# Optimization experiments

Hardware: AMD Instinct MI355X
Metric: run time of the kernel (lower is better)

The kernel has to match this reference:

```python
import jax, jax.numpy as jnp
import numpy as np

TAU = 0.3  # default tau in selectCom_adap
K = 1      # hard-coded K in selectCom_adap

B, C, N, M = 8, 64, 2048, 2048


def setup_inputs() -> dict:
    key = jax.random.key(0)
    k1, k2, k3, k4 = jax.random.split(key, 4)
    return {
        "src_emb": jax.random.normal(k1, (B, C, N), dtype=jnp.float32),
        "tgt_emb": jax.random.normal(k2, (B, C, M), dtype=jnp.float32),
        "src": jax.random.normal(k3, (B, 3, N), dtype=jnp.float32),
        "tgt": jax.random.normal(k4, (B, 3, M), dtype=jnp.float32),
    }


def reference(src_emb, tgt_emb, src, tgt):
    # EPCOR eval path: selectCom_adap + get_sparse_w
    dtype = src_emb.dtype
    Np = src_emb.shape[2]
    Mp = tgt_emb.shape[2]
    tgt_K = int(Mp * TAU)
    src_K = int(Np * TAU)

    inner = jnp.einsum('bcn,bcm->bnm', src_emb, tgt_emb)
    xx = jnp.sum(src_emb * src_emb, axis=1)[:, :, None]   # [B,N,1]
    yy = jnp.sum(tgt_emb * tgt_emb, axis=1)[:, None, :]   # [B,1,M]
    pd = 2.0 * inner - xx - yy                             # [B,N,M]

    # column softmax and tgt outlier mask (smallest tgt_K column mass)
    scoresSoftCol = jax.nn.softmax(pd, axis=2)
    scoresColSum = jnp.sum(scoresSoftCol, axis=1)          # [B,M]
    col_thresh = -jax.lax.top_k(-scoresColSum, tgt_K)[0][:, -1]  # tgt_K-th smallest, [B]
    mask_tgt = (scoresColSum < col_thresh[:, None])[:, None, :]  # [B,1,M]

    # row softmax and src outlier mask (smallest src_K row mass)
    scoresSoftRow = jax.nn.softmax(pd, axis=1)
    scoresRowSum = jnp.sum(scoresSoftRow, axis=2)          # [B,N]
    row_thresh = -jax.lax.top_k(-scoresRowSum, src_K)[0][:, -1]  # [B]
    mask_src = (scoresRowSum < row_thresh[:, None])[:, :, None]  # [B,N,1]

    mask = jnp.logical_or(mask_src, mask_tgt)              # [B,N,M]

    # torch precedence: mask = (mask + scoresSoftCol) < topk  (bool promoted to float)
    topk = jax.lax.top_k(scoresSoftCol, K)[0][..., -1:]    # K-th largest per row, [B,N,1]
    mask = (mask.astype(dtype) + scoresSoftCol) < topk     # [B,N,M]

    w_sparse = jnp.where(mask, jnp.zeros((), dtype), scoresSoftCol)
    colsum = jnp.sum(w_sparse, axis=-1, keepdims=True)
    colsum = jnp.where(colsum < 1e-5, jnp.asarray(1e-5, dtype), colsum)
    src_tgt_weight = w_sparse / colsum                     # row-renormalized sparse weights

    val_sum = jnp.sum(src_tgt_weight, axis=-1, keepdims=True)  # [B,N,1]
    val_sum_inlier = jnp.where(mask_src, jnp.zeros((), dtype), val_sum)[..., 0]  # [B,N]
    src_weight = val_sum_inlier / jnp.sum(val_sum_inlier, axis=-1, keepdims=True)

    # src_corr = tgt @ src_tgt_weight^T : [B,3,M] x [B,N,M] -> [B,3,N]
    src_corr = jnp.einsum('bdm,bnm->bdn', tgt, src_tgt_weight)
    return src_corr, src_weight, mask_src, mask_tgt
```

## Files before the change

### kernel.cpp

```cpp
#include <hip/hip_runtime.h>

#define BB 8
#define CC 64
#define NN 2048
#define MM 2048
#define KSEL 613
#define MT 32
#define MT2 16
#define NT2 16
#define NCH 16

#define OUT_W  (BB * 3 * NN)
#define OUT_MS (OUT_W + BB * NN)
#define OUT_MT (OUT_MS + BB * NN)

typedef __bf16 bf16x8 __attribute__((ext_vector_type(8)));
typedef float f32x4 __attribute__((ext_vector_type(4)));
typedef unsigned short u16;

#define MFMA16 __builtin_amdgcn_mfma_f32_16x16x32_bf16

__device__ __forceinline__ void split3(float a, u16& u0, u16& u1, u16& u2) {
    __bf16 h0 = (__bf16)a; float f0 = (float)h0;
    float r1 = a - f0;
    __bf16 h1 = (__bf16)r1; float f1 = (float)h1;
    float r2 = r1 - f1;
    __bf16 h2 = (__bf16)r2;
    u0 = __builtin_bit_cast(u16, h0);
    u1 = __builtin_bit_cast(u16, h1);
    u2 = __builtin_bit_cast(u16, h2);
}

__global__ __launch_bounds__(256) void split_k(const float* __restrict__ E,
                                               float* __restrict__ sq,
                                               unsigned* __restrict__ T0,
                                               unsigned* __restrict__ T1,
                                               unsigned* __restrict__ T2) {
    __shared__ float Ls[64][65];
    __shared__ float sacc[64];
    int b = blockIdx.y, n0 = blockIdx.x * 64, t = threadIdx.x;
    const float* Eb = E + (size_t)b * CC * NN + n0;
#pragma unroll
    for (int i = 0; i < 4; ++i) {
        int idx = (i << 8) + t, c = idx >> 4, nq = idx & 15;
        float4 v = *(const float4*)(Eb + (size_t)c * NN + (nq << 2));
        Ls[c][nq * 4 + 0] = v.x; Ls[c][nq * 4 + 1] = v.y;
        Ls[c][nq * 4 + 2] = v.z; Ls[c][nq * 4 + 3] = v.w;
    }
    __syncthreads();
    int j = t & 31, nn = t >> 5;
#pragma unroll
    for (int p = 0; p < 8; ++p) {
        int n = (p << 3) + nn;
        float a = Ls[2 * j][n], c = Ls[2 * j + 1][n];
        float s = a * a + c * c;
#pragma unroll
        for (int d = 1; d < 32; d <<= 1) s += __shfl_xor(s, d);
        if (j == 0) sacc[n] = s;
        u16 a0, a1, a2, c0, c1, c2;
        split3(a, a0, a1, a2);
        split3(c, c0, c1, c2);
        size_t row = (size_t)(b * NN + n0 + n) * 32 + j;
        T0[row] = (unsigned)a0 | ((unsigned)c0 << 16);
        T1[row] = (unsigned)a1 | ((unsigned)c1 << 16);
        T2[row] = (unsigned)a2 | ((unsigned)c2 << 16);
    }
    __syncthreads();
    if (t < 64) sq[b * NN + n0 + t] = sacc[t];
}

__device__ __forceinline__ void stage_tile(u16* dst, const unsigned* src,
                                           int base_nm, int kc, int t) {
#pragma unroll
    for (int i = 0; i < 2; ++i) {
        int d = (((i << 8) + t) << 4);
        int nn_ = d >> 6, c4 = (d >> 4) & 3;
        const char* gs = (const char*)src + ((size_t)(base_nm + nn_) << 7) +
                         ((size_t)kc << 6) + ((c4 ^ ((nn_ >> 1) & 3)) << 4);
        __builtin_amdgcn_global_load_lds(
            (const __attribute__((address_space(1))) void*)gs,
            (__attribute__((address_space(3))) void*)((char*)dst + d), 16, 0, 0);
    }
}

__device__ __forceinline__ bf16x8 frag(const u16* tile, int nloc, int g) {
    return *(const bf16x8*)((const char*)tile + (nloc << 6) + ((g ^ ((nloc >> 1) & 3)) << 4));
}

__global__ __launch_bounds__(256, 3) void gemm_pd_k(
    const unsigned* __restrict__ A0, const unsigned* __restrict__ A1, const unsigned* __restrict__ A2,
    const unsigned* __restrict__ B0, const unsigned* __restrict__ B1, const unsigned* __restrict__ B2,
    const float* __restrict__ xx, const float* __restrict__ yy,
    float* __restrict__ pd,
    float* __restrict__ rpM, float* __restrict__ rpS,
    float* __restrict__ cpM, float* __restrict__ cpS) {
    __shared__ u16 Ta0[128 * 32], Tb0[128 * 32], Tax[128 * 32], Tbx[128 * 32];
    __shared__ float rowm2[2][128], rows2[2][128];
    __shared__ float colm2[2][128], cols2[2][128];
    int flat = blockIdx.x + (blockIdx.y << 4) + (blockIdx.z << 8);
    int b = flat & 7, rest = flat >> 3;
    int mt = rest & 15, nt = rest >> 4;
    int n0 = nt << 7;
    int m0 = mt << 7;
    int t = threadIdx.x, lane = t & 63, w = t >> 6;
    int wn = w >> 1, wm = w & 1;
    int g = lane >> 4, q = lane & 15;
    int baseA = b * NN + n0, baseB = b * MM + m0;

    f32x4 acc[4][4] = {};

#pragma unroll
    for (int kc = 0; kc < 2; ++kc) {
        stage_tile(Ta0, A0, baseA, kc, t);
        stage_tile(Tb0, B0, baseB, kc, t);
        stage_tile(Tax, A1, baseA, kc, t);
        stage_tile(Tbx, B1, baseB, kc, t);
        __syncthreads();
        bf16x8 fa0[4], fb0[4], fax[4], fbx[4];
#pragma unroll
        for (int i = 0; i < 4; ++i) {
            fa0[i] = frag(Ta0, wn * 64 + i * 16 + q, g);
            fb0[i] = frag(Tb0, wm * 64 + i * 16 + q, g);
            fax[i] = frag(Tax, wn * 64 + i * 16 + q, g);
            fbx[i] = frag(Tbx, wm * 64 + i * 16 + q, g);
        }
#pragma unroll
        for (int mg = 0; mg < 4; ++mg)
#pragma unroll
            for (int ng = 0; ng < 4; ++ng)
                acc[ng][mg] = MFMA16(fa0[ng], fb0[mg], acc[ng][mg], 0, 0, 0);
#pragma unroll
        for (int mg = 0; mg < 4; ++mg)
#pragma unroll
            for (int ng = 0; ng < 4; ++ng)
                acc[ng][mg] = MFMA16(fa0[ng], fbx[mg], acc[ng][mg], 0, 0, 0);
#pragma unroll
        for (int mg = 0; mg < 4; ++mg)
#pragma unroll
            for (int ng = 0; ng < 4; ++ng)
                acc[ng][mg] = MFMA16(fax[ng], fb0[mg], acc[ng][mg], 0, 0, 0);
#pragma unroll
        for (int mg = 0; mg < 4; ++mg)
#pragma unroll
            for (int ng = 0; ng < 4; ++ng)
                acc[ng][mg] = MFMA16(fax[ng], fbx[mg], acc[ng][mg], 0, 0, 0);
        __syncthreads();
        stage_tile(Tax, A2, baseA, kc, t);
        stage_tile(Tbx, B2, baseB, kc, t);
        __syncthreads();
#pragma unroll
        for (int i = 0; i < 4; ++i) {
            fax[i] = frag(Tax, wn * 64 + i * 16 + q, g);
            fbx[i] = frag(Tbx, wm * 64 + i * 16 + q, g);
        }
#pragma unroll
        for (int mg = 0; mg < 4; ++mg)
#pragma unroll
            for (int ng = 0; ng < 4; ++ng)
                acc[ng][mg] = MFMA16(fa0[ng], fbx[mg], acc[ng][mg], 0, 0, 0);
#pragma unroll
        for (int mg = 0; mg < 4; ++mg)
#pragma unroll
            for (int ng = 0; ng < 4; ++ng)
                acc[ng][mg] = MFMA16(fax[ng], fb0[mg], acc[ng][mg], 0, 0, 0);
        __syncthreads();
    }

    int nbase = n0 + wn * 64;
    int mbase = m0 + wm * 64;
    float xv[4][4];
#pragma unroll
    for (int ng = 0; ng < 4; ++ng)
#pragma unroll
        for (int r = 0; r < 4; ++r)
            xv[ng][r] = xx[b * NN + nbase + ng * 16 + g * 4 + r];
    float yv[4];
#pragma unroll
    for (int mg = 0; mg < 4; ++mg) yv[mg] = yy[b * MM + mbase + mg * 16 + q];

#pragma unroll
    for (int ng = 0; ng < 4; ++ng)
#pragma unroll
        for (int r = 0; r < 4; ++r) {
            float* prow = pd + ((size_t)(b * NN + nbase + ng * 16 + g * 4 + r)) * MM + mbase + q;
#pragma unroll
            for (int mg = 0; mg < 4; ++mg) {
                float o = 2.f * acc[ng][mg][r] - xv[ng][r] - yv[mg];
                acc[ng][mg][r] = o;
                prow[mg * 16] = o;
            }
        }

#pragma unroll
    for (int ng = 0; ng < 4; ++ng)
#pragma unroll
        for (int r = 0; r < 4; ++r) {
            float mx = fmaxf(fmaxf(acc[ng][0][r], acc[ng][1][r]),
                             fmaxf(acc[ng][2][r], acc[ng][3][r]));
#pragma unroll
            for (int d = 1; d < 16; d <<= 1) mx = fmaxf(mx, __shfl_xor(mx, d));
            float s = __expf(acc[ng][0][r] - mx) + __expf(acc[ng][1][r] - mx) +
                      __expf(acc[ng][2][r] - mx) + __expf(acc[ng][3][r] - mx);
#pragma unroll
            for (int d = 1; d < 16; d <<= 1) s += __shfl_xor(s, d);
            if (q == 0) {
                int nl = wn * 64 + ng * 16 + g * 4 + r;
                rowm2[wm][nl] = mx;
                rows2[wm][nl] = s;
            }
        }

#pragma unroll
    for (int mg = 0; mg < 4; ++mg) {
        float cx = -3.4e38f;
#pragma unroll
        for (int ng = 0; ng < 4; ++ng)
#pragma unroll
            for (int r = 0; r < 4; ++r) cx = fmaxf(cx, acc[ng][mg][r]);
        cx = fmaxf(cx, __shfl_xor(cx, 16));
        cx = fmaxf(cx, __shfl_xor(cx, 32));
        float cs = 0.f;
#pragma unroll
        for (int ng = 0; ng < 4; ++ng)
#pragma unroll
            for (int r = 0; r < 4; ++r) cs += __expf(acc[ng][mg][r] - cx);
        cs += __shfl_xor(cs, 16);
        cs += __shfl_xor(cs, 32);
        if (lane < 16) {
            int ml = wm * 64 + mg * 16 + q;
            colm2[wn][ml] = cx;
            cols2[wn][ml] = cs;
        }
    }
    __syncthreads();

    if (t < 128) {
        float ma = rowm2[0][t], mb = rowm2[1][t];
        float M = fmaxf(ma, mb);
        float S = rows2[0][t] * __expf(ma - M) + rows2[1][t] * __expf(mb - M);
        size_t base = ((size_t)(b * MT2 + mt)) * NN + n0 + t;
        rpM[base] = M;
        rpS[base] = S;
    } else {
        int m = t - 128;
        float ma = colm2[0][m], mb = colm2[1][m];
        float M = fmaxf(ma, mb);
        float S = cols2[0][m] * __expf(ma - M) + cols2[1][m] * __expf(mb - M);
        size_t base = ((size_t)(b * NT2 + nt)) * MM + m0 + m;
        cpM[base] = M;
        cpS[base] = S;
    }
}

__global__ __launch_bounds__(256) void comb_rc_k(const float* __restrict__ rpM,
                                                 const float* __restrict__ rpS,
                                                 const float* __restrict__ cpM,
                                                 const float* __restrict__ cpS,
                                                 float* __restrict__ rowmax,
                                                 float* __restrict__ rowsum,
                                                 float* __restrict__ colmax,
                                                 float* __restrict__ colsum) {
    int b = blockIdx.y, which = blockIdx.z;
    int i = blockIdx.x * 256 + threadIdx.x;
    const float* pM = which ? cpM : rpM;
    const float* pS = which ? cpS : rpS;
    float* oM = which ? colmax : rowmax;
    float* oS = which ? colsum : rowsum;
    float Mv = -3.4e38f;
#pragma unroll
    for (int k = 0; k < 16; ++k) Mv = fmaxf(Mv, pM[(size_t)(b * 16 + k) * 2048 + i]);
    float S = 0.f;
#pragma unroll
    for (int k = 0; k < 16; ++k) {
        size_t o = (size_t)(b * 16 + k) * 2048 + i;
        S += pS[o] * __expf(pM[o] - Mv);
    }
    oM[b * 2048 + i] = Mv;
    oS[b * 2048 + i] = S;
}

__global__ __launch_bounds__(256) void cross_k(const float* __restrict__ pd,
                                               const float* __restrict__ rowmax,
                                               const float* __restrict__ rowsum,
                                               const float* __restrict__ colmax,
                                               const float* __restrict__ colsum,
                                               float* __restrict__ sRowp,
                                               float* __restrict__ sColp) {
    __shared__ float rmx[128], rin[128];
    __shared__ float rowpart[128][65];
    __shared__ float colacc[4][64];
    int b = blockIdx.z, nc = blockIdx.y, mtile = blockIdx.x;
    int m0 = mtile << 6;
    int t = threadIdx.x, mL = t & 63, ng = t >> 6;
    if (t < 128) {
        int n = nc * 128 + t;
        rmx[t] = rowmax[b * NN + n];
        rin[t] = 1.f / rowsum[b * NN + n];
    }
    float cmv = colmax[b * MM + m0 + mL];
    float civ = 1.f / colsum[b * MM + m0 + mL];
    __syncthreads();
    const float* base = pd + ((size_t)(b * NN + nc * 128)) * MM + m0 + mL;
    float scp = 0.f;
#pragma unroll
    for (int i = 0; i < 32; ++i) {
        int nl = (i << 2) + ng;
        float v = base[(size_t)nl * MM];
        scp += __expf(v - rmx[nl]) * rin[nl];
        rowpart[nl][mL] = __expf(v - cmv) * civ;
    }
    colacc[ng][mL] = scp;
    __syncthreads();
    if (t < 128) {
        float s = 0.f;
#pragma unroll
        for (int c = 0; c < 64; ++c) s += rowpart[t][c];
        sRowp[((size_t)(b * MT + mtile)) * NN + nc * 128 + t] = s;
    } else if (t < 192) {
        int m = t - 128;
        sColp[((size_t)(b * NCH + nc)) * MM + m0 + m] =
            colacc[0][m] + colacc[1][m] + colacc[2][m] + colacc[3][m];
    }
}

__global__ __launch_bounds__(256) void comb_s_k(const float* __restrict__ sRowp,
                                                const float* __restrict__ sColp,
                                                float* __restrict__ sRow,
                                                float* __restrict__ sCol) {
    int b = blockIdx.y, which = blockIdx.z;
    int i = blockIdx.x * 256 + threadIdx.x;
    if (!which) {
        float s = 0.f;
#pragma unroll
        for (int k = 0; k < MT; ++k) s += sRowp[(size_t)(b * MT + k) * NN + i];
        sRow[b * NN + i] = s;
    } else {
        float s = 0.f;
#pragma unroll
        for (int k = 0; k < NCH; ++k) s += sColp[(size_t)(b * NCH + k) * MM + i];
        sCol[b * MM + i] = s;
    }
}

__global__ __launch_bounds__(64) void select_k(const float* __restrict__ sRow,
                                               const float* __restrict__ sCol,
                                               float* __restrict__ rth,
                                               float* __restrict__ cth) {
    int kind = blockIdx.x, b = blockIdx.y, t = threadIdx.x;
    const float* vals = (kind == 0) ? (sRow + b * NN) : (sCol + b * MM);
    float v[32];
#pragma unroll
    for (int i = 0; i < 32; ++i) v[i] = vals[t + (i << 6)];
    unsigned lo = 0u, hi = 0x7F800000u;
    while (lo < hi) {
        unsigned mid = lo + ((hi - lo) >> 1);
        float pv = __uint_as_float(mid);
        int c = 0;
#pragma unroll
        for (int i = 0; i < 32; ++i) c += (v[i] <= pv) ? 1 : 0;
#pragma unroll
        for (int off = 32; off > 0; off >>= 1) c += __shfl_down(c, off);
        c = __shfl(c, 0);
        if (c >= KSEL + 1) hi = mid; else lo = mid + 1;
    }
    if (t == 0) { if (kind == 0) rth[b] = __uint_as_float(lo); else cth[b] = __uint_as_float(lo); }
}

__global__ __launch_bounds__(256) void masks_k(const float* __restrict__ sRow,
                                               const float* __restrict__ sCol,
                                               const float* __restrict__ rth,
                                               const float* __restrict__ cth,
                                               float* __restrict__ out) {
    int b = blockIdx.x, t = threadIdx.x;
    float r = rth[b], c = cth[b];
    int cnt = 0;
    bool ms[8];
#pragma unroll
    for (int i = 0; i < 8; ++i) {
        int n = t + (i << 8);
        ms[i] = sRow[b * NN + n] < r;
        out[OUT_MS + b * NN + n] = ms[i] ? 1.f : 0.f;
        out[OUT_MT + b * MM + n] = (sCol[b * MM + n] < c) ? 1.f : 0.f;
        cnt += ms[i] ? 0 : 1;
    }
#pragma unroll
    for (int off = 32; off > 0; off >>= 1) cnt += __shfl_down(cnt, off);
    __shared__ int wcnt[4];
    int wave = t >> 6, lane = t & 63;
    if (lane == 0) wcnt[wave] = cnt;
    __syncthreads();
    float inv = 1.f / (float)(wcnt[0] + wcnt[1] + wcnt[2] + wcnt[3]);
#pragma unroll
    for (int i = 0; i < 8; ++i) {
        int n = t + (i << 8);
        out[OUT_W + b * NN + n] = ms[i] ? 0.f : inv;
    }
}

__global__ __launch_bounds__(256) void corr_k(const float* __restrict__ pd,
                                              const float* __restrict__ rowmax,
                                              const float* __restrict__ rowsum,
                                              const float* __restrict__ sRow,
                                              const float* __restrict__ sCol,
                                              const float* __restrict__ rth,
                                              const float* __restrict__ cth,
                                              const float* __restrict__ tgt,
                                              float* __restrict__ out) {
    int b = blockIdx.y;
    int n = (blockIdx.x << 2) + (threadIdx.x >> 6);
    int lane = threadIdx.x & 63;
    const float4* row4 = (const float4*)(pd + ((size_t)b * NN + n) * MM);
    const float4* sc4 = (const float4*)(sCol + b * MM);
    const float4* tg4 = (const float4*)(tgt + (size_t)b * 3 * MM);
    float rmax = rowmax[b * NN + n];
    float rsum = rowsum[b * NN + n];
    float cthv = cth[b];
    bool msrc = sRow[b * NN + n] < rth[b];
    float cs = 0.f, d0 = 0.f, d1 = 0.f, d2 = 0.f;
#pragma unroll
    for (int g = 0; g < 8; ++g) {
        int j = lane + (g << 6);
        float p[4], sc[4], t0[4], t1[4], t2[4];
        *(float4*)p = row4[j];
        *(float4*)sc = sc4[j];
        *(float4*)t0 = tg4[j];
        *(float4*)t1 = tg4[j + MM / 4];
        *(float4*)t2 = tg4[j + MM / 2];
#pragma unroll
        for (int c = 0; c < 4; ++c) {
            bool keep = msrc || (sc[c] < cthv) || (p[c] == rmax);
            if (keep) {
                float s = __expf(p[c] - rmax) / rsum;
                cs += s;
                d0 += s * t0[c];
                d1 += s * t1[c];
                d2 += s * t2[c];
            }
        }
    }
#pragma unroll
    for (int off = 32; off > 0; off >>= 1) {
        cs += __shfl_down(cs, off);
        d0 += __shfl_down(d0, off);
        d1 += __shfl_down(d1, off);
        d2 += __shfl_down(d2, off);
    }
    if (lane == 0) {
        cs = (cs < 1e-5f) ? 1e-5f : cs;
        out[(b * 3 + 0) * NN + n] = d0 / cs;
        out[(b * 3 + 1) * NN + n] = d1 / cs;
        out[(b * 3 + 2) * NN + n] = d2 / cs;
    }
}

extern "C" void kernel_launch(void* const* d_in, const int* in_sizes, int n_in,
                              void* d_out, int out_size, void* d_ws, size_t ws_size,
                              hipStream_t stream) {
    const float* src_emb = (const float*)d_in[0];
    const float* tgt_emb = (const float*)d_in[1];
    const float* tgt = (const float*)d_in[3];
    float* out = (float*)d_out;

    float* ws = (float*)d_ws;
    float* pd     = ws;
    float* xx     = pd + (size_t)BB * NN * MM;
    float* yy     = xx + BB * NN;
    float* rowmax = yy + BB * MM;
    float* rowsum = rowmax + BB * NN;
    float* colmax = rowsum + BB * NN;
    float* colsum = colmax + BB * MM;
    float* sRow   = colsum + BB * MM;
    float* sCol   = sRow + BB * NN;
    float* rth    = sCol + BB * MM;
    float* cth    = rth + BB;
    float* rpM    = cth + BB;
    float* rpS    = rpM + (size_t)BB * 16 * NN;
    float* cpM    = rpS + (size_t)BB * 16 * NN;
    float* cpS    = cpM + (size_t)BB * 16 * MM;
    float* sRowp  = cpS + (size_t)BB * 16 * MM;
    float* sColp  = sRowp + (size_t)BB * MT * NN;
    unsigned* At0 = (unsigned*)(sColp + (size_t)BB * NCH * MM);
    unsigned* At1 = At0 + (size_t)BB * NN * 32;
    unsigned* At2 = At1 + (size_t)BB * NN * 32;
    unsigned* Bt0 = At2 + (size_t)BB * NN * 32;
    unsigned* Bt1 = Bt0 + (size_t)BB * MM * 32;
    unsigned* Bt2 = Bt1 + (size_t)BB * MM * 32;

    split_k<<<dim3(NN / 64, BB), 256, 0, stream>>>(src_emb, xx, At0, At1, At2);
    split_k<<<dim3(MM / 64, BB), 256, 0, stream>>>(tgt_emb, yy, Bt0, Bt1, Bt2);
    gemm_pd_k<<<dim3(16, 16, BB), 256, 0, stream>>>(At0, At1, At2, Bt0, Bt1, Bt2,
                                                    xx, yy, pd, rpM, rpS, cpM, cpS);
    comb_rc_k<<<dim3(2048 / 256, BB, 2), 256, 0, stream>>>(rpM, rpS, cpM, cpS,
                                                           rowmax, rowsum, colmax, colsum);
    cross_k<<<dim3(MT, NCH, BB), 256, 0, stream>>>(pd, rowmax, rowsum, colmax, colsum, sRowp, sColp);
    comb_s_k<<<dim3(2048 / 256, BB, 2), 256, 0, stream>>>(sRowp, sColp, sRow, sCol);
    select_k<<<dim3(2, BB), 64, 0, stream>>>(sRow, sCol, rth, cth);
    masks_k<<<dim3(BB), 256, 0, stream>>>(sRow, sCol, rth, cth, out);
    corr_k<<<dim3(NN / 4, BB), 256, 0, stream>>>(pd, rowmax, rowsum, sRow, sCol, rth, cth, tgt, out);
}
```

Measured before the change: 195.9 us.

## Stage all split tiles at once in GEMM and split mask kernel

The GEMM kernel now holds all three split-precision tiles for A and B in shared memory and loads them together. This drops the mid-iteration barrier pair and the re-staging of the third split, at the cost of more LDS per block, which may reduce occupancy at the 3-blocks-per-CU launch bound. Separately, the masks kernel is spread over 4 blocks per batch with a new weight kernel that reduces the partial counts. This raises parallelism for that tail step but adds one more kernel launch.

```diff
diff --git a/kernel.cpp b/kernel.cpp
--- a/kernel.cpp
+++ b/kernel.cpp
@@ -94,7 +94,8 @@
     float* __restrict__ pd,
     float* __restrict__ rpM, float* __restrict__ rpS,
     float* __restrict__ cpM, float* __restrict__ cpS) {
-    __shared__ u16 Ta0[128 * 32], Tb0[128 * 32], Tax[128 * 32], Tbx[128 * 32];
+    __shared__ u16 Ta0[128 * 32], Ta1[128 * 32], Ta2[128 * 32];
+    __shared__ u16 Tb0[128 * 32], Tb1[128 * 32], Tb2[128 * 32];
     __shared__ float rowm2[2][128], rows2[2][128];
     __shared__ float colm2[2][128], cols2[2][128];
     int flat = blockIdx.x + (blockIdx.y << 4) + (blockIdx.z << 8);
@@ -113,16 +114,18 @@
     for (int kc = 0; kc < 2; ++kc) {
         stage_tile(Ta0, A0, baseA, kc, t);
         stage_tile(Tb0, B0, baseB, kc, t);
-        stage_tile(Tax, A1, baseA, kc, t);
-        stage_tile(Tbx, B1, baseB, kc, t);
+        stage_tile(Ta1, A1, baseA, kc, t);
+        stage_tile(Tb1, B1, baseB, kc, t);
+        stage_tile(Ta2, A2, baseA, kc, t);
+        stage_tile(Tb2, B2, baseB, kc, t);
         __syncthreads();
         bf16x8 fa0[4], fb0[4], fax[4], fbx[4];
 #pragma unroll
         for (int i = 0; i < 4; ++i) {
             fa0[i] = frag(Ta0, wn * 64 + i * 16 + q, g);
             fb0[i] = frag(Tb0, wm * 64 + i * 16 + q, g);
-            fax[i] = frag(Tax, wn * 64 + i * 16 + q, g);
-            fbx[i] = frag(Tbx, wm * 64 + i * 16 + q, g);
+            fax[i] = frag(Ta1, wn * 64 + i * 16 + q, g);
+            fbx[i] = frag(Tb1, wm * 64 + i * 16 + q, g);
         }
 #pragma unroll
         for (int mg = 0; mg < 4; ++mg)
@@ -144,14 +147,10 @@
 #pragma unroll
             for (int ng = 0; ng < 4; ++ng)
                 acc[ng][mg] = MFMA16(fax[ng], fbx[mg], acc[ng][mg], 0, 0, 0);
-        __syncthreads();
-        stage_tile(Tax, A2, baseA, kc, t);
-        stage_tile(Tbx, B2, baseB, kc, t);
-        __syncthreads();
 #pragma unroll
         for (int i = 0; i < 4; ++i) {
-            fax[i] = frag(Tax, wn * 64 + i * 16 + q, g);
-            fbx[i] = frag(Tbx, wm * 64 + i * 16 + q, g);
+            fax[i] = frag(Ta2, wn * 64 + i * 16 + q, g);
+            fbx[i] = frag(Tb2, wm * 64 + i * 16 + q, g);
         }
 #pragma unroll
         for (int mg = 0; mg < 4; ++mg)
@@ -370,14 +369,15 @@
                                                const float* __restrict__ sCol,
                                                const float* __restrict__ rth,
                                                const float* __restrict__ cth,
-                                               float* __restrict__ out) {
-    int b = blockIdx.x, t = threadIdx.x;
+                                               float* __restrict__ out,
+                                               int* __restrict__ cntP) {
+    int b = blockIdx.y, qd = blockIdx.x, t = threadIdx.x;
     float r = rth[b], c = cth[b];
     int cnt = 0;
-    bool ms[8];
-#pragma unroll
-    for (int i = 0; i < 8; ++i) {
-        int n = t + (i << 8);
+    bool ms[2];
+#pragma unroll
+    for (int i = 0; i < 2; ++i) {
+        int n = (qd << 9) + (i << 8) + t;
         ms[i] = sRow[b * NN + n] < r;
         out[OUT_MS + b * NN + n] = ms[i] ? 1.f : 0.f;
         out[OUT_MT + b * MM + n] = (sCol[b * MM + n] < c) ? 1.f : 0.f;
@@ -389,11 +389,20 @@
     int wave = t >> 6, lane = t & 63;
     if (lane == 0) wcnt[wave] = cnt;
     __syncthreads();
-    float inv = 1.f / (float)(wcnt[0] + wcnt[1] + wcnt[2] + wcnt[3]);
-#pragma unroll
-    for (int i = 0; i < 8; ++i) {
-        int n = t + (i << 8);
-        out[OUT_W + b * NN + n] = ms[i] ? 0.f : inv;
+    if (t == 0) cntP[b * 4 + qd] = wcnt[0] + wcnt[1] + wcnt[2] + wcnt[3];
+}
+
+__global__ __launch_bounds__(256) void weight_k(const float* __restrict__ sRow,
+                                                const float* __restrict__ rth,
+                                                const int* __restrict__ cntP,
+                                                float* __restrict__ out) {
+    int b = blockIdx.y, qd = blockIdx.x, t = threadIdx.x;
+    float r = rth[b];
+    float inv = 1.f / (float)(cntP[b * 4] + cntP[b * 4 + 1] + cntP[b * 4 + 2] + cntP[b * 4 + 3]);
+#pragma unroll
+    for (int i = 0; i < 2; ++i) {
+        int n = (qd << 9) + (i << 8) + t;
+        out[OUT_W + b * NN + n] = (sRow[b * NN + n] < r) ? 0.f : inv;
     }
 }
 
@@ -473,7 +482,8 @@
     float* sCol   = sRow + BB * NN;
     float* rth    = sCol + BB * MM;
     float* cth    = rth + BB;
-    float* rpM    = cth + BB;
+    int*   cntP   = (int*)(cth + BB);
+    float* rpM    = (float*)(cntP + BB * 4);
     float* rpS    = rpM + (size_t)BB * 16 * NN;
     float* cpM    = rpS + (size_t)BB * 16 * NN;
     float* cpS    = cpM + (size_t)BB * 16 * MM;
@@ -495,6 +505,7 @@
     cross_k<<<dim3(MT, NCH, BB), 256, 0, stream>>>(pd, rowmax, rowsum, colmax, colsum, sRowp, sColp);
     comb_s_k<<<dim3(2048 / 256, BB, 2), 256, 0, stream>>>(sRowp, sColp, sRow, sCol);
     select_k<<<dim3(2, BB), 64, 0, stream>>>(sRow, sCol, rth, cth);
-    masks_k<<<dim3(BB), 256, 0, stream>>>(sRow, sCol, rth, cth, out);
+    masks_k<<<dim3(4, BB), 256, 0, stream>>>(sRow, sCol, rth, cth, out, cntP);
+    weight_k<<<dim3(4, BB), 256, 0, stream>>>(sRow, rth, cntP, out);
     corr_k<<<dim3(NN / 4, BB), 256, 0, stream>>>(pd, rowmax, rowsum, sRow, sCol, rth, cth, tgt, out);
 }
```

After: 204.5 us. 1.04x slower.
